# Optimization experiments

Hardware: AMD Instinct MI355X
Metric: run time of the kernel (lower is better)

The kernel has to match this reference:

```python
import jax, jax.numpy as jnp
import numpy as np

N_NODES = 100000
K_HOPS = 10
ALPHA = 0.1


def gcn_conv(x, src, dst, W, b, num_nodes):
    # GCNConv: linear first (cheaper: out_dim small), then D^-1/2 (A+I) D^-1/2 aggregation
    h = x @ W  # [N, out]
    deg = jax.ops.segment_sum(jnp.ones_like(dst, dtype=h.dtype), dst, num_segments=num_nodes)
    dinv = jnp.where(deg > 0, jax.lax.rsqrt(deg), 0.0)
    norm = dinv[src] * dinv[dst]  # [E]
    msg = h[src] * norm[:, None]
    out = jax.ops.segment_sum(msg, dst, num_segments=num_nodes)
    return out + b


def _with_self_loops(edge_index, num_nodes):
    loops = jnp.arange(num_nodes, dtype=edge_index.dtype)
    src = jnp.concatenate([edge_index[0], loops])
    dst = jnp.concatenate([edge_index[1], loops])
    return src, dst


def setup_inputs() -> dict:
    key = jax.random.key(0)
    ks = jax.random.split(key, 8)
    n_feat, hidden, n_cls, n_edges = 512, 16, 7, 3200000
    x = jax.random.normal(ks[0], (N_NODES, n_feat), dtype=jnp.float32)
    edge_index = jax.random.randint(ks[1], (2, n_edges), 0, N_NODES, dtype=jnp.int64)
    W1 = jax.random.normal(ks[2], (n_feat, hidden), dtype=jnp.float32) * 0.05
    b1 = jnp.zeros((hidden,), dtype=jnp.float32)
    Wl = jax.random.normal(ks[3], (hidden, hidden), dtype=jnp.float32) * 0.25
    bl = jnp.zeros((hidden,), dtype=jnp.float32)
    W2 = jax.random.normal(ks[4], (hidden, n_cls), dtype=jnp.float32) * 0.25
    b2 = jnp.zeros((n_cls,), dtype=jnp.float32)
    return {"x": x, "edge_index": edge_index, "W1": W1, "b1": b1, "Wl": Wl, "bl": bl, "W2": W2, "b2": b2}


def reference(x, edge_index, W1, b1, Wl, bl, W2, b2):
    src, dst = _with_self_loops(edge_index, N_NODES)
    h = jax.nn.relu(gcn_conv(x, src, dst, W1, b1, N_NODES))
    def body(h, _):
        h = ALPHA * jax.nn.relu(h @ Wl + bl) + (1.0 - ALPHA) * h
        return h, None
    h, _ = jax.lax.scan(body, h, None, length=K_HOPS)
    out = gcn_conv(h, src, dst, W2, b2, N_NODES)
    return jax.nn.log_softmax(out, axis=1)
```

## Files before the change

kernel.cpp:

```cpp
#include <hip/hip_runtime.h>
#include <math.h>

#define N_NODES 100000
#define N_EDGES 3200000
#define F_IN    512
#define HID     16
#define NCLS    7
#define ALPHA   0.1f
#define K_HOPS  10

#define SHIFT   7
#define BWIDTH  128
#define NBUCK   ((N_NODES + BWIDTH - 1) / BWIDTH)
#define SLAB    5120
#define CHUNK   4096
#define BIN_T   512
#define EPT     (CHUNK / BIN_T)
#define A3_BLOCKS ((N_EDGES + CHUNK - 1) / CHUNK)

#define OFF_BCUR    0u
#define OFF_RP      1024u
#define OFF_DEG     101376u
#define OFF_DINV    201728u
#define OFF_COL     302080u
#define OFF_BINNED  4305920u
#define OFF_H0      8309760u
#define OFF_Z       9909760u

__global__ void __launch_bounds__(BIN_T)
k_bin(const int* __restrict__ src, const int* __restrict__ dst,
      int* __restrict__ bcur, unsigned int* __restrict__ binned) {
    __shared__ int ha[NBUCK];
    __shared__ int gbase[NBUCK];
    __shared__ int lcur[NBUCK];
    int tid = threadIdx.x;
    int e0 = blockIdx.x * CHUNK;
    int e1 = e0 + CHUNK;
    if (e1 > N_EDGES) e1 = N_EDGES;
    for (int i = tid; i < NBUCK; i += BIN_T) ha[i] = 0;
    __syncthreads();
    int dloc[EPT];
#pragma unroll
    for (int i = 0; i < EPT; i++) {
        int e = e0 + tid + i * BIN_T;
        dloc[i] = (e < e1) ? dst[e] : -1;
        if (dloc[i] >= 0) atomicAdd(&ha[dloc[i] >> SHIFT], 1);
    }
    __syncthreads();
    for (int s = tid; s < NBUCK; s += BIN_T) {
        int c = ha[s];
        lcur[s] = 0;
        gbase[s] = c ? (s * SLAB + atomicAdd(&bcur[s], c)) : 0;
    }
    __syncthreads();
#pragma unroll
    for (int i = 0; i < EPT; i++) {
        int d = dloc[i];
        if (d >= 0) {
            int e = e0 + tid + i * BIN_T;
            int bk = d >> SHIFT;
            int idx = atomicAdd(&lcur[bk], 1);
            binned[gbase[bk] + idx] =
                ((unsigned int)(d & (BWIDTH - 1)) << 17) | (unsigned int)src[e];
        }
    }
}

__global__ void __launch_bounds__(512)
k_csr(const unsigned int* __restrict__ binned, const int* __restrict__ bcur,
      int* __restrict__ rp, int* __restrict__ deg, float* __restrict__ dinv,
      int* __restrict__ col) {
    __shared__ int cnt[BWIDTH];
    __shared__ int s[BWIDTH];
    __shared__ int cur[BWIDTH];
    int tid = threadIdx.x;
    int b = blockIdx.x;
    int base = b << SHIFT;
    int e0 = b * SLAB;
    int e1 = e0 + bcur[b];
    if (tid < BWIDTH) cnt[tid] = 0;
    __syncthreads();
    for (int e = e0 + tid; e < e1; e += 512)
        atomicAdd(&cnt[binned[e] >> 17], 1);
    __syncthreads();
    int v = 0;
    if (tid < BWIDTH) { v = cnt[tid]; s[tid] = v; }
    __syncthreads();
    for (int off = 1; off < BWIDTH; off <<= 1) {
        int t = 0;
        if (tid < BWIDTH && tid >= off) t = s[tid - off];
        __syncthreads();
        if (tid < BWIDTH) s[tid] += t;
        __syncthreads();
    }
    if (tid < BWIDTH) {
        int ex = s[tid] - v;
        cur[tid] = ex;
        int node = base + tid;
        if (node < N_NODES) {
            rp[node] = e0 + ex;
            deg[node] = v;
            dinv[node] = rsqrtf((float)(v + 1));
        }
    }
    __syncthreads();
    for (int e = e0 + tid; e < e1; e += 512) {
        unsigned int w = binned[e];
        int ln = (int)(w >> 17);
        int p = atomicAdd(&cur[ln], 1);
        col[e0 + p] = (int)(w & 0x1FFFFu);
    }
}

#define XWN_BLOCKS 512
#define XWN_WAVES  (XWN_BLOCKS * 4)

__device__ __forceinline__ float4 shfl4_xor(float4 v, int m) {
    float4 r;
    r.x = __shfl_xor(v.x, m);
    r.y = __shfl_xor(v.y, m);
    r.z = __shfl_xor(v.z, m);
    r.w = __shfl_xor(v.w, m);
    return r;
}
__device__ __forceinline__ float4 add4(float4 a, float4 b) {
    a.x += b.x; a.y += b.y; a.z += b.z; a.w += b.w;
    return a;
}

__global__ void __launch_bounds__(256)
k_xw1(const float* __restrict__ x, const float* __restrict__ W,
      const float* __restrict__ dinv, float* __restrict__ h0s) {
    int lane = threadIdx.x & 63;
    int wid = (blockIdx.x * 256 + threadIdx.x) >> 6;

    float4 w[32];
    const float4* W4 = (const float4*)W;
#pragma unroll
    for (int j = 0; j < 8; j++) {
#pragma unroll
        for (int q = 0; q < 4; q++)
            w[j * 4 + q] = W4[(8 * lane + j) * 4 + q];
    }

    int node = wid;
    float4 xc0, xc1, xn0, xn1;
    if (node < N_NODES) {
        const float4* xr = (const float4*)(x + (size_t)node * F_IN) + 2 * lane;
        xc0 = xr[0];
        xc1 = xr[1];
    }
    int n1 = node + XWN_WAVES;
    if (n1 < N_NODES) {
        const float4* xr = (const float4*)(x + (size_t)n1 * F_IN) + 2 * lane;
        xn0 = xr[0];
        xn1 = xr[1];
    }

    for (; node < N_NODES; node += XWN_WAVES) {
        int n2 = node + 2 * XWN_WAVES;
        float4 xp0, xp1;
        if (n2 < N_NODES) {
            const float4* xr = (const float4*)(x + (size_t)n2 * F_IN) + 2 * lane;
            xp0 = xr[0];
            xp1 = xr[1];
        }

        float xa0 = xc0.x, xa1 = xc0.y, xa2 = xc0.z, xa3 = xc0.w;
        float xa4 = xc1.x, xa5 = xc1.y, xa6 = xc1.z, xa7 = xc1.w;

        float4 pp0 = make_float4(0.f, 0.f, 0.f, 0.f);
        float4 pp1 = pp0, pp2 = pp0, pp3 = pp0;
#define XW_FMA(J, XA)                                            \
        pp0.x += XA * w[J*4+0].x; pp0.y += XA * w[J*4+0].y;      \
        pp0.z += XA * w[J*4+0].z; pp0.w += XA * w[J*4+0].w;      \
        pp1.x += XA * w[J*4+1].x; pp1.y += XA * w[J*4+1].y;      \
        pp1.z += XA * w[J*4+1].z; pp1.w += XA * w[J*4+1].w;      \
        pp2.x += XA * w[J*4+2].x; pp2.y += XA * w[J*4+2].y;      \
        pp2.z += XA * w[J*4+2].z; pp2.w += XA * w[J*4+2].w;      \
        pp3.x += XA * w[J*4+3].x; pp3.y += XA * w[J*4+3].y;      \
        pp3.z += XA * w[J*4+3].z; pp3.w += XA * w[J*4+3].w;
        XW_FMA(0, xa0) XW_FMA(1, xa1) XW_FMA(2, xa2) XW_FMA(3, xa3)
        XW_FMA(4, xa4) XW_FMA(5, xa5) XW_FMA(6, xa6) XW_FMA(7, xa7)
#undef XW_FMA

        int b5 = (lane >> 5) & 1;
        float4 k0 = b5 ? pp2 : pp0;
        float4 k1 = b5 ? pp3 : pp1;
        float4 s0 = b5 ? pp0 : pp2;
        float4 s1 = b5 ? pp1 : pp3;
        k0 = add4(k0, shfl4_xor(s0, 32));
        k1 = add4(k1, shfl4_xor(s1, 32));

        int b4 = (lane >> 4) & 1;
        float4 kk = b4 ? k1 : k0;
        float4 ss = b4 ? k0 : k1;
        kk = add4(kk, shfl4_xor(ss, 16));

        int b3 = (lane >> 3) & 1;
        float e0 = b3 ? kk.z : kk.x;
        float e1 = b3 ? kk.w : kk.y;
        float f0 = b3 ? kk.x : kk.z;
        float f1 = b3 ? kk.y : kk.w;
        e0 += __shfl_xor(f0, 8);
        e1 += __shfl_xor(f1, 8);

        int b2 = (lane >> 2) & 1;
        float v = b2 ? e1 : e0;
        float sv = b2 ? e0 : e1;
        v += __shfl_xor(sv, 4);

        v += __shfl_xor(v, 1);
        v += __shfl_xor(v, 2);

        if ((lane & 3) == 0) {
            float dv = dinv[node];
            h0s[(size_t)node * HID + (lane >> 2)] = dv * v;
        }

        xc0 = xn0; xc1 = xn1;
        xn0 = xp0; xn1 = xp1;
    }
}

__global__ void k_agg1hops(const float* __restrict__ h0s, const int* __restrict__ rp,
                           const int* __restrict__ deg, const int* __restrict__ col,
                           const float* __restrict__ dinv, const float* __restrict__ b1,
                           const float* __restrict__ Wl, const float* __restrict__ bl,
                           const float* __restrict__ W2, float* __restrict__ zs) {
    int node = (blockIdx.x * blockDim.x + threadIdx.x) >> 6;
    if (node >= N_NODES) return;
    int lane = threadIdx.x & 63;
    int c = lane & 15, eo = lane >> 4;
    int e0 = rp[node], e1 = e0 + deg[node];
    float acc = 0.f;
    int e = e0 + eo;
    for (; e + 12 < e1; e += 16) {
        int c0 = col[e];
        int c1 = col[e + 4];
        int c2 = col[e + 8];
        int c3 = col[e + 12];
        float v0 = h0s[(size_t)c0 * HID + c];
        float v1 = h0s[(size_t)c1 * HID + c];
        float v2 = h0s[(size_t)c2 * HID + c];
        float v3 = h0s[(size_t)c3 * HID + c];
        acc += v0;
        acc += v1;
        acc += v2;
        acc += v3;
    }
    for (; e + 4 < e1; e += 8) {
        int c0 = col[e];
        int c1 = col[e + 4];
        float v0 = h0s[(size_t)c0 * HID + c];
        float v1 = h0s[(size_t)c1 * HID + c];
        acc += v0;
        acc += v1;
    }
    if (e < e1) acc += h0s[(size_t)col[e] * HID + c];
    acc += __shfl_xor(acc, 16);
    acc += __shfl_xor(acc, 32);

    float dv = dinv[node];
    float o = dv * (acc + h0s[(size_t)node * HID + c]) + b1[c];
    float h = fmaxf(o, 0.f);

    int bs = lane & 48;
    for (int it = 0; it < K_HOPS; it++) {
        float tm = bl[c];
#pragma unroll
        for (int k = 0; k < HID; k++) {
            float hk = __shfl(h, bs + k);
            tm += hk * Wl[k * HID + c];
        }
        h = ALPHA * fmaxf(tm, 0.f) + (1.f - ALPHA) * h;
    }

    float zz = 0.f;
#pragma unroll
    for (int k = 0; k < HID; k++) {
        float hk = __shfl(h, bs + k);
        float w2v = (c < NCLS) ? W2[k * NCLS + c] : 0.f;
        zz += hk * w2v;
    }
    if (eo == 0 && c < 8) zs[(size_t)node * 8 + c] = dv * zz;
}

__global__ void k_agg2(const float* __restrict__ zs, const int* __restrict__ rp,
                       const int* __restrict__ deg, const int* __restrict__ col,
                       const float* __restrict__ dinv, const float* __restrict__ b2,
                       float* __restrict__ out) {
    int node = (blockIdx.x * blockDim.x + threadIdx.x) >> 6;
    if (node >= N_NODES) return;
    int lane = threadIdx.x & 63;
    int c = lane & 7, eo = lane >> 3;
    int e0 = rp[node], e1 = e0 + deg[node];
    float acc = 0.f;
    int e = e0 + eo;
    for (; e + 24 < e1; e += 32) {
        int c0 = col[e];
        int c1 = col[e + 8];
        int c2 = col[e + 16];
        int c3 = col[e + 24];
        float v0 = zs[(size_t)c0 * 8 + c];
        float v1 = zs[(size_t)c1 * 8 + c];
        float v2 = zs[(size_t)c2 * 8 + c];
        float v3 = zs[(size_t)c3 * 8 + c];
        acc += v0;
        acc += v1;
        acc += v2;
        acc += v3;
    }
    for (; e + 8 < e1; e += 16) {
        int c0 = col[e];
        int c1 = col[e + 8];
        float v0 = zs[(size_t)c0 * 8 + c];
        float v1 = zs[(size_t)c1 * 8 + c];
        acc += v0;
        acc += v1;
    }
    if (e < e1) acc += zs[(size_t)col[e] * 8 + c];
    acc += __shfl_xor(acc, 8);
    acc += __shfl_xor(acc, 16);
    acc += __shfl_xor(acc, 32);
    float o = dinv[node] * (acc + zs[(size_t)node * 8 + c]) + ((c < NCLS) ? b2[c] : 0.f);
    float val = (c < NCLS) ? o : -INFINITY;
    float m = val;
    m = fmaxf(m, __shfl_xor(m, 1));
    m = fmaxf(m, __shfl_xor(m, 2));
    m = fmaxf(m, __shfl_xor(m, 4));
    float ex = (c < NCLS) ? expf(o - m) : 0.f;
    float ss = ex;
    ss += __shfl_xor(ss, 1);
    ss += __shfl_xor(ss, 2);
    ss += __shfl_xor(ss, 4);
    if (eo == 0 && c < NCLS) out[(size_t)node * NCLS + c] = o - m - logf(ss);
}

extern "C" void kernel_launch(void* const* d_in, const int* in_sizes, int n_in,
                              void* d_out, int out_size, void* d_ws, size_t ws_size,
                              hipStream_t stream) {
    const float* x  = (const float*)d_in[0];
    const int*   ei = (const int*)d_in[1];
    const float* W1 = (const float*)d_in[2];
    const float* b1 = (const float*)d_in[3];
    const float* Wl = (const float*)d_in[4];
    const float* bl = (const float*)d_in[5];
    const float* W2 = (const float*)d_in[6];
    const float* b2 = (const float*)d_in[7];
    float* out = (float*)d_out;

    int*   wsI = (int*)d_ws;
    float* wsF = (float*)d_ws;
    int*          bcur   = wsI + OFF_BCUR;
    int*          rp     = wsI + OFF_RP;
    int*          deg    = wsI + OFF_DEG;
    float*        dinv   = wsF + OFF_DINV;
    int*          col    = wsI + OFF_COL;
    unsigned int* binned = (unsigned int*)(wsI + OFF_BINNED);
    float*        h0s    = wsF + OFF_H0;
    float*        zs     = wsF + OFF_Z;

    const int* src = ei;
    const int* dst = ei + N_EDGES;

    hipMemsetAsync(bcur, 0, NBUCK * sizeof(int), stream);

    k_bin<<<A3_BLOCKS, BIN_T, 0, stream>>>(src, dst, bcur, binned);
    k_csr<<<NBUCK, 512, 0, stream>>>(binned, bcur, rp, deg, dinv, col);
    k_xw1<<<XWN_BLOCKS, 256, 0, stream>>>(x, W1, dinv, h0s);
    k_agg1hops<<<(N_NODES * 64 + 255) / 256, 256, 0, stream>>>(h0s, rp, deg, col, dinv,
                                                               b1, Wl, bl, W2, zs);
    k_agg2<<<(N_NODES * 64 + 255) / 256, 256, 0, stream>>>(zs, rp, deg, col, dinv, b2, out);
}
```

Before: 644.3 us.

## Map four nodes per wavefront in layer-1 aggregation and add bounds guards

The first aggregation kernel now gives each 16-lane group its own node instead of spreading one node's edges across a whole wavefront. This cuts the launched grid by four and drops the cross-group shuffle reduction. Wl and W2 columns are hoisted into registers ahead of the hop loop. Bounds clamps are also added on slab fill, degree and the binned write position, and uninitialised float4 registers in the x@W1 kernel are zeroed. Per-node serial edge loops may load-imbalance across groups within a wave and give less memory parallelism per node.

```diff
diff --git a/kernel.cpp b/kernel.cpp
--- a/kernel.cpp
+++ b/kernel.cpp
@@ -60,8 +60,10 @@
             int e = e0 + tid + i * BIN_T;
             int bk = d >> SHIFT;
             int idx = atomicAdd(&lcur[bk], 1);
-            binned[gbase[bk] + idx] =
-                ((unsigned int)(d & (BWIDTH - 1)) << 17) | (unsigned int)src[e];
+            int pos = gbase[bk] + idx;
+            if (pos < (int)(NBUCK * SLAB))
+                binned[pos] =
+                    ((unsigned int)(d & (BWIDTH - 1)) << 17) | (unsigned int)src[e];
         }
     }
 }
@@ -77,7 +79,9 @@
     int b = blockIdx.x;
     int base = b << SHIFT;
     int e0 = b * SLAB;
-    int e1 = e0 + bcur[b];
+    int fill = bcur[b];
+    if (fill > SLAB) fill = SLAB;
+    int e1 = e0 + fill;
     if (tid < BWIDTH) cnt[tid] = 0;
     __syncthreads();
     for (int e = e0 + tid; e < e1; e += 512)
@@ -143,8 +147,9 @@
             w[j * 4 + q] = W4[(8 * lane + j) * 4 + q];
     }
 
+    float4 z4 = make_float4(0.f, 0.f, 0.f, 0.f);
     int node = wid;
-    float4 xc0, xc1, xn0, xn1;
+    float4 xc0 = z4, xc1 = z4, xn0 = z4, xn1 = z4;
     if (node < N_NODES) {
         const float4* xr = (const float4*)(x + (size_t)node * F_IN) + 2 * lane;
         xc0 = xr[0];
@@ -159,7 +164,7 @@
 
     for (; node < N_NODES; node += XWN_WAVES) {
         int n2 = node + 2 * XWN_WAVES;
-        float4 xp0, xp1;
+        float4 xp0 = z4, xp1 = z4;
         if (n2 < N_NODES) {
             const float4* xr = (const float4*)(x + (size_t)n2 * F_IN) + 2 * lane;
             xp0 = xr[0];
@@ -169,8 +174,7 @@
         float xa0 = xc0.x, xa1 = xc0.y, xa2 = xc0.z, xa3 = xc0.w;
         float xa4 = xc1.x, xa5 = xc1.y, xa6 = xc1.z, xa7 = xc1.w;
 
-        float4 pp0 = make_float4(0.f, 0.f, 0.f, 0.f);
-        float4 pp1 = pp0, pp2 = pp0, pp3 = pp0;
+        float4 pp0 = z4, pp1 = z4, pp2 = z4, pp3 = z4;
 #define XW_FMA(J, XA)                                            \
         pp0.x += XA * w[J*4+0].x; pp0.y += XA * w[J*4+0].y;      \
         pp0.z += XA * w[J*4+0].z; pp0.w += XA * w[J*4+0].w;      \
@@ -223,55 +227,60 @@
     }
 }
 
-__global__ void k_agg1hops(const float* __restrict__ h0s, const int* __restrict__ rp,
-                           const int* __restrict__ deg, const int* __restrict__ col,
-                           const float* __restrict__ dinv, const float* __restrict__ b1,
-                           const float* __restrict__ Wl, const float* __restrict__ bl,
-                           const float* __restrict__ W2, float* __restrict__ zs) {
-    int node = (blockIdx.x * blockDim.x + threadIdx.x) >> 6;
+__global__ void __launch_bounds__(256)
+k_agg1hops(const float* __restrict__ h0s, const int* __restrict__ rp,
+           const int* __restrict__ deg, const int* __restrict__ col,
+           const float* __restrict__ dinv, const float* __restrict__ b1,
+           const float* __restrict__ Wl, const float* __restrict__ bl,
+           const float* __restrict__ W2, float* __restrict__ zs) {
+    int lane = threadIdx.x & 63;
+    int grp = lane >> 4;
+    int c = lane & 15;
+    int node = ((blockIdx.x * 256 + threadIdx.x) >> 6) * 4 + grp;
     if (node >= N_NODES) return;
-    int lane = threadIdx.x & 63;
-    int c = lane & 15, eo = lane >> 4;
-    int e0 = rp[node], e1 = e0 + deg[node];
-    float acc = 0.f;
-    int e = e0 + eo;
-    for (; e + 12 < e1; e += 16) {
+
+    int e0 = rp[node];
+    int dg = deg[node];
+    if (dg < 0) dg = 0;
+    if (dg > SLAB) dg = SLAB;
+    int e1 = e0 + dg;
+
+    float acc0 = 0.f, acc1 = 0.f, acc2 = 0.f, acc3 = 0.f;
+    for (int e = e0; e < e1; e += 4) {
         int c0 = col[e];
-        int c1 = col[e + 4];
-        int c2 = col[e + 8];
-        int c3 = col[e + 12];
+        bool m1 = (e + 1 < e1), m2 = (e + 2 < e1), m3 = (e + 3 < e1);
+        int c1 = m1 ? col[e + 1] : 0;
+        int c2 = m2 ? col[e + 2] : 0;
+        int c3 = m3 ? col[e + 3] : 0;
         float v0 = h0s[(size_t)c0 * HID + c];
-        float v1 = h0s[(size_t)c1 * HID + c];
-        float v2 = h0s[(size_t)c2 * HID + c];
-        float v3 = h0s[(size_t)c3 * HID + c];
-        acc += v0;
-        acc += v1;
-        acc += v2;
-        acc += v3;
-    }
-    for (; e + 4 < e1; e += 8) {
-        int c0 = col[e];
-        int c1 = col[e + 4];
-        float v0 = h0s[(size_t)c0 * HID + c];
-        float v1 = h0s[(size_t)c1 * HID + c];
-        acc += v0;
-        acc += v1;
-    }
-    if (e < e1) acc += h0s[(size_t)col[e] * HID + c];
-    acc += __shfl_xor(acc, 16);
-    acc += __shfl_xor(acc, 32);
+        float v1 = m1 ? h0s[(size_t)c1 * HID + c] : 0.f;
+        float v2 = m2 ? h0s[(size_t)c2 * HID + c] : 0.f;
+        float v3 = m3 ? h0s[(size_t)c3 * HID + c] : 0.f;
+        acc0 += v0;
+        acc1 += v1;
+        acc2 += v2;
+        acc3 += v3;
+    }
+    float acc = (acc0 + acc1) + (acc2 + acc3);
 
     float dv = dinv[node];
     float o = dv * (acc + h0s[(size_t)node * HID + c]) + b1[c];
     float h = fmaxf(o, 0.f);
 
+    float w[HID], w2[HID];
+#pragma unroll
+    for (int k = 0; k < HID; k++) w[k] = Wl[k * HID + c];
+#pragma unroll
+    for (int k = 0; k < HID; k++) w2[k] = (c < NCLS) ? W2[k * NCLS + c] : 0.f;
+    float blc = bl[c];
+
     int bs = lane & 48;
     for (int it = 0; it < K_HOPS; it++) {
-        float tm = bl[c];
+        float tm = blc;
 #pragma unroll
         for (int k = 0; k < HID; k++) {
             float hk = __shfl(h, bs + k);
-            tm += hk * Wl[k * HID + c];
+            tm += hk * w[k];
         }
         h = ALPHA * fmaxf(tm, 0.f) + (1.f - ALPHA) * h;
     }
@@ -280,10 +289,9 @@
 #pragma unroll
     for (int k = 0; k < HID; k++) {
         float hk = __shfl(h, bs + k);
-        float w2v = (c < NCLS) ? W2[k * NCLS + c] : 0.f;
-        zz += hk * w2v;
-    }
-    if (eo == 0 && c < 8) zs[(size_t)node * 8 + c] = dv * zz;
+        zz += hk * w2[k];
+    }
+    if (c < 8) zs[(size_t)node * 8 + c] = dv * zz;
 }
 
 __global__ void k_agg2(const float* __restrict__ zs, const int* __restrict__ rp,
@@ -294,7 +302,11 @@
     if (node >= N_NODES) return;
     int lane = threadIdx.x & 63;
     int c = lane & 7, eo = lane >> 3;
-    int e0 = rp[node], e1 = e0 + deg[node];
+    int e0 = rp[node];
+    int dg = deg[node];
+    if (dg < 0) dg = 0;
+    if (dg > SLAB) dg = SLAB;
+    int e1 = e0 + dg;
     float acc = 0.f;
     int e = e0 + eo;
     for (; e + 24 < e1; e += 32) {
@@ -369,7 +381,7 @@
     k_bin<<<A3_BLOCKS, BIN_T, 0, stream>>>(src, dst, bcur, binned);
     k_csr<<<NBUCK, 512, 0, stream>>>(binned, bcur, rp, deg, dinv, col);
     k_xw1<<<XWN_BLOCKS, 256, 0, stream>>>(x, W1, dinv, h0s);
-    k_agg1hops<<<(N_NODES * 64 + 255) / 256, 256, 0, stream>>>(h0s, rp, deg, col, dinv,
-                                                               b1, Wl, bl, W2, zs);
+    k_agg1hops<<<(N_NODES / 4 * 64) / 256, 256, 0, stream>>>(h0s, rp, deg, col, dinv,
+                                                             b1, Wl, bl, W2, zs);
     k_agg2<<<(N_NODES * 64 + 255) / 256, 256, 0, stream>>>(zs, rp, deg, col, dinv, b2, out);
 }
```

After: 525.9 us. 1.23x faster.
